# Performance work log

Hardware: AMD Instinct MI355X
Metric: run time of the kernel (lower is better)

## Reference

```python
import jax, jax.numpy as jnp
import numpy as np

N_NODES = 200000


def setup_inputs() -> dict:
    key = jax.random.key(0)
    k1, k2, k3, k4 = jax.random.split(key, 4)
    x = jax.random.normal(k1, (N_NODES, 16), dtype=jnp.float32)
    edge_index = jax.random.randint(k2, (2, 2400000), 0, N_NODES, dtype=jnp.int64)
    W1 = jax.random.normal(k3, (16, 32), dtype=jnp.float32) * 0.25
    b1 = jnp.zeros((32,), dtype=jnp.float32)
    W2 = jax.random.normal(k4, (32, 32), dtype=jnp.float32) * 0.18
    b2 = jnp.zeros((32,), dtype=jnp.float32)
    return {"x": x, "edge_index": edge_index, "W1": W1, "b1": b1, "W2": W2, "b2": b2}


def _gcn_norm(edge_index, n_nodes):
    # Add self-loops (GCNConv default) and compute symmetric normalization
    # norm[e] = deg(src)^-1/2 * deg(dst)^-1/2 over A + I.
    loop = jnp.arange(n_nodes, dtype=edge_index.dtype)
    src = jnp.concatenate([edge_index[0], loop])
    dst = jnp.concatenate([edge_index[1], loop])
    deg = jax.ops.segment_sum(jnp.ones_like(dst, dtype=jnp.float32), dst,
                              num_segments=n_nodes)
    dinv = jax.lax.rsqrt(deg)  # deg >= 1 thanks to self-loops
    norm = dinv[src] * dinv[dst]  # [E + N]
    return src, dst, norm


def _gcn_layer(h, src, dst, norm, W, b, n_nodes):
    m = h @ W                      # [N, out] dense transform first (fewer bytes moved)
    agg = jax.ops.segment_sum(m[src] * norm[:, None], dst, num_segments=n_nodes)
    return agg + b


def reference(x, edge_index, W1, b1, W2, b2):
    n = x.shape[0]
    src, dst, norm = _gcn_norm(edge_index, n)
    h = jax.nn.relu(_gcn_layer(x, src, dst, norm, W1, b1, n))
    out = _gcn_layer(h, src, dst, norm, W2, b2, n)
    return out
```

## Files before the change

### kernel.cpp

```cpp
#include <hip/hip_runtime.h>

#define TPB 256
#define BEB 2048
#define SEB 2048
#define PEB 8192
#define NS_SH 7
#define NS (1 << NS_SH)
#define CAP3 4096

__global__ void k_detect_i64(const unsigned int* __restrict__ ei, int E,
                             int* __restrict__ flag, int* __restrict__ cum) {
  __shared__ int nz;
  if (threadIdx.x == 0) nz = 0;
  if (threadIdx.x < 7) cum[threadIdx.x] = 0;
  __syncthreads();
  int step = E / 4096;
  if (step < 1) step = 1;
  for (int t = threadIdx.x; t < 4096; t += blockDim.x) {
    long long pos = 1 + 2LL * (long long)t * step;
    if (pos < 2LL * (long long)E && ei[pos] != 0u) atomicAdd(&nz, 1);
  }
  __syncthreads();
  if (threadIdx.x == 0) *flag = (nz == 0) ? 1 : 0;
}

__device__ __forceinline__ int load_idx(const void* __restrict__ p, long long pos,
                                        int is64) {
  if (is64) return (int)(((const long long*)p)[pos]);
  return ((const int*)p)[pos];
}

__global__ void k_zero_i(int* __restrict__ p, int n) {
  int i = blockIdx.x * blockDim.x + threadIdx.x;
  if (i < n) p[i] = 0;
}

__global__ void k_count8(const void* __restrict__ ei, const int* __restrict__ flag,
                         int* __restrict__ cum, int E, int Nc) {
  int is64 = *flag;
  int c[7] = {0, 0, 0, 0, 0, 0, 0};
  int stride = gridDim.x * blockDim.x;
  for (int e = blockIdx.x * blockDim.x + threadIdx.x; e < E; e += stride) {
    int d = load_idx(ei, (long long)E + e, is64);
#pragma unroll
    for (int k = 0; k < 7; ++k) c[k] += (d < (k + 1) * Nc) ? 1 : 0;
  }
#pragma unroll
  for (int k = 0; k < 7; ++k)
#pragma unroll
    for (int off = 32; off >= 1; off >>= 1) c[k] += __shfl_xor(c[k], off);
  __shared__ int red[4][7];
  int lane = threadIdx.x & 63, wid = threadIdx.x >> 6;
  if (lane == 0) {
#pragma unroll
    for (int k = 0; k < 7; ++k) red[wid][k] = c[k];
  }
  __syncthreads();
  if (threadIdx.x < 7) {
    int s = red[0][threadIdx.x] + red[1][threadIdx.x] +
            red[2][threadIdx.x] + red[3][threadIdx.x];
    if (s) atomicAdd(&cum[threadIdx.x], s);
  }
}

__global__ void k_cbase(const int* __restrict__ cum, int* __restrict__ ccnt,
                        int* __restrict__ cbase, int* __restrict__ gtail, int E) {
  if (threadIdx.x == 0) {
    int prev = 0, acc = 0;
    for (int g = 0; g < 8; ++g) {
      int cg = ((g < 7) ? cum[g] : E) - prev;
      prev = (g < 7) ? cum[g] : E;
      ccnt[g] = cg;
      cbase[g] = acc;
      gtail[g] = acc;
      acc += cg;
    }
  }
}

__global__ void k_bucket(const void* __restrict__ ei, const int* __restrict__ flag,
                         int* __restrict__ gtail, unsigned long long* __restrict__ pair,
                         int E, int Nc) {
  __shared__ int sd[BEB], ss[BEB];
  __shared__ int bbase[8], cur[8];
  __shared__ int red[4][7];
  int is64 = *flag;
  int base = blockIdx.x * BEB;
  int cnt = min(BEB, E - base);
  int c[7] = {0, 0, 0, 0, 0, 0, 0};
  for (int i = threadIdx.x; i < cnt; i += TPB) {
    int e = base + i;
    int d = load_idx(ei, (long long)E + e, is64);
    int s = load_idx(ei, e, is64);
    sd[i] = d;
    ss[i] = s;
#pragma unroll
    for (int k = 0; k < 7; ++k) c[k] += (d < (k + 1) * Nc) ? 1 : 0;
  }
#pragma unroll
  for (int k = 0; k < 7; ++k)
#pragma unroll
    for (int off = 32; off >= 1; off >>= 1) c[k] += __shfl_xor(c[k], off);
  int lane = threadIdx.x & 63, wid = threadIdx.x >> 6;
  if (lane == 0) {
#pragma unroll
    for (int k = 0; k < 7; ++k) red[wid][k] = c[k];
  }
  __syncthreads();
  if (threadIdx.x < 8) {
    int g = threadIdx.x;
    int hi = (g < 7) ? (red[0][g] + red[1][g] + red[2][g] + red[3][g]) : cnt;
    int lo = (g > 0) ? (red[0][g - 1] + red[1][g - 1] + red[2][g - 1] + red[3][g - 1]) : 0;
    bbase[g] = atomicAdd(&gtail[g], hi - lo);
    cur[g] = 0;
  }
  __syncthreads();
  int trips = (cnt + TPB - 1) / TPB;
  unsigned long long lt = (1ULL << lane) - 1ULL;
  for (int t = 0; t < trips; ++t) {
    int i = t * TPB + threadIdx.x;
    bool act = i < cnt;
    int d = act ? sd[i] : 0;
    int s = act ? ss[i] : 0;
    int g = 0;
#pragma unroll
    for (int k = 1; k <= 7; ++k) g += (d >= k * Nc) ? 1 : 0;
    unsigned long long m0 = __ballot(act && g == 0);
    unsigned long long m1 = __ballot(act && g == 1);
    unsigned long long m2 = __ballot(act && g == 2);
    unsigned long long m3 = __ballot(act && g == 3);
    unsigned long long m4 = __ballot(act && g == 4);
    unsigned long long m5 = __ballot(act && g == 5);
    unsigned long long m6 = __ballot(act && g == 6);
    unsigned long long m7 = __ballot(act && g == 7);
    int wb = 0;
    if (lane < 8) {
      unsigned long long mm =
          lane < 4 ? (lane < 2 ? (lane == 0 ? m0 : m1) : (lane == 2 ? m2 : m3))
                   : (lane < 6 ? (lane == 4 ? m4 : m5) : (lane == 6 ? m6 : m7));
      wb = atomicAdd(&cur[lane], (int)__popcll(mm));
    }
    int mybase = __shfl(wb, g);
    unsigned long long mk =
        g < 4 ? (g < 2 ? (g == 0 ? m0 : m1) : (g == 2 ? m2 : m3))
              : (g < 6 ? (g == 4 ? m4 : m5) : (g == 6 ? m6 : m7));
    int rank = (int)__popcll(mk & lt);
    if (act) {
      int pos = bbase[g] + mybase + rank;
      unsigned long long pk =
          ((unsigned long long)(unsigned)s << 32) | (unsigned)d;
      __builtin_nontemporal_store(pk, &pair[pos]);
    }
  }
}

__global__ void k_scnt(const int* __restrict__ cbase, const int* __restrict__ ccnt,
                       const int2* __restrict__ pair, int* __restrict__ scnt,
                       int nsb_c, int Nc) {
  __shared__ int hist[256];
  for (int t = threadIdx.x; t < nsb_c; t += TPB) hist[t] = 0;
  __syncthreads();
  int g = blockIdx.x & 7, seg = blockIdx.x >> 3;
  int cnt = ccnt[g];
  int base = seg * SEB;
  if (base < cnt) {
    int lim = min(base + SEB, cnt);
    const int2* pp = pair + cbase[g];
    int lo = g * Nc;
    for (int i = base + threadIdx.x; i < lim; i += TPB)
      atomicAdd(&hist[(pp[i].x - lo) >> NS_SH], 1);
  }
  __syncthreads();
  for (int t = threadIdx.x; t < nsb_c; t += TPB)
    if (hist[t]) atomicAdd(&scnt[g * nsb_c + t], hist[t]);
}

__global__ void k_sbase(const int* __restrict__ scnt, int* __restrict__ sbase,
                        int* __restrict__ stail, int nsb) {
  __shared__ int p[1024];
  int t = threadIdx.x;
  int i0 = 2 * t, i1 = 2 * t + 1;
  int v0 = (i0 < nsb) ? scnt[i0] : 0;
  int v1 = (i1 < nsb) ? scnt[i1] : 0;
  p[t] = v0 + v1;
  __syncthreads();
#pragma unroll
  for (int off = 1; off < 1024; off <<= 1) {
    int u = (t >= off) ? p[t - off] : 0;
    __syncthreads();
    p[t] += u;
    __syncthreads();
  }
  int excl = p[t] - (v0 + v1);
  if (i0 < nsb) { sbase[i0] = excl; stail[i0] = excl; }
  if (i1 < nsb) { sbase[i1] = excl + v0; stail[i1] = excl + v0; }
}

__global__ void k_place2(const int* __restrict__ cbase, const int* __restrict__ ccnt,
                         const unsigned long long* __restrict__ pair,
                         int* __restrict__ stail, unsigned long long* __restrict__ pair2,
                         int nsb_c, int Nc) {
  __shared__ unsigned long long sorted[PEB];
  __shared__ int hist[256], bb[256], gb[256], cur[256];
  int g = blockIdx.x & 7, seg = blockIdx.x >> 3;
  int cnt = ccnt[g];
  int base = seg * PEB;
  if (base >= cnt) return;
  int lim = min(base + PEB, cnt);
  int lo = g * Nc;
  const unsigned long long* pp = pair + cbase[g];
  for (int t = threadIdx.x; t < 256; t += TPB) hist[t] = 0;
  __syncthreads();
  for (int i = base + threadIdx.x; i < lim; i += TPB) {
    int d = (int)(unsigned)(pp[i] & 0xffffffffULL);
    atomicAdd(&hist[(d - lo) >> NS_SH], 1);
  }
  __syncthreads();
  {
    int t = threadIdx.x;
    int v = hist[t];
    bb[t] = v;
    __syncthreads();
#pragma unroll
    for (int off = 1; off < 256; off <<= 1) {
      int u = (t >= off) ? bb[t - off] : 0;
      __syncthreads();
      bb[t] += u;
      __syncthreads();
    }
    bb[t] -= v;
  }
  for (int t = threadIdx.x; t < nsb_c; t += TPB) {
    gb[t] = hist[t] ? atomicAdd(&stail[g * nsb_c + t], hist[t]) : 0;
    cur[t] = 0;
  }
  __syncthreads();
  for (int i = base + threadIdx.x; i < lim; i += TPB) {
    unsigned long long pk = pp[i];
    int d = (int)(unsigned)(pk & 0xffffffffULL);
    int sb = (d - lo) >> NS_SH;
    int r = atomicAdd(&cur[sb], 1);
    sorted[bb[sb] + r] = pk;
  }
  __syncthreads();
  int n = lim - base;
  for (int i = threadIdx.x; i < n; i += TPB) {
    unsigned long long pk = sorted[i];
    int d = (int)(unsigned)(pk & 0xffffffffULL);
    int sb = (d - lo) >> NS_SH;
    pair2[gb[sb] + (i - bb[sb])] = pk;
  }
}

__global__ void k_hist3(const int* __restrict__ scnt, const int* __restrict__ sbase,
                        const int2* __restrict__ pair2, int* __restrict__ degi,
                        int nsb_c, int Nc, int N) {
  __shared__ int hist[NS];
  int sb = blockIdx.x;
  int g = sb / nsb_c, lsb = sb - g * nsb_c;
  int n0 = g * Nc + (lsb << NS_SH);
  int nn = min(NS, min(Nc - (lsb << NS_SH), N - n0));
  if (nn <= 0) return;
  for (int t = threadIdx.x; t < NS; t += TPB) hist[t] = 0;
  __syncthreads();
  int cnt = scnt[sb];
  const int2* pp = pair2 + sbase[sb];
  for (int i = threadIdx.x; i < cnt; i += TPB) atomicAdd(&hist[pp[i].x - n0], 1);
  __syncthreads();
  for (int t = threadIdx.x; t < nn; t += TPB) degi[n0 + t] = hist[t];
}

__global__ void k_scan1(const int* __restrict__ degi, int* __restrict__ incl,
                        int* __restrict__ bsums, int n) {
  __shared__ int s[TPB];
  int i = blockIdx.x * TPB + threadIdx.x;
  int v = (i < n) ? degi[i] : 0;
  s[threadIdx.x] = v;
  __syncthreads();
#pragma unroll
  for (int off = 1; off < TPB; off <<= 1) {
    int t = (threadIdx.x >= off) ? s[threadIdx.x - off] : 0;
    __syncthreads();
    s[threadIdx.x] += t;
    __syncthreads();
  }
  if (i < n) incl[i] = s[threadIdx.x];
  if (threadIdx.x == TPB - 1) bsums[blockIdx.x] = s[TPB - 1];
}

__global__ void k_scan2(int* __restrict__ bsums, int nb) {
  __shared__ int s[1024];
  int t = threadIdx.x;
  int v = (t < nb) ? bsums[t] : 0;
  s[t] = v;
  __syncthreads();
#pragma unroll
  for (int off = 1; off < 1024; off <<= 1) {
    int u = (t >= off) ? s[t - off] : 0;
    __syncthreads();
    s[t] += u;
    __syncthreads();
  }
  if (t < nb) bsums[t] = s[t] - v;
}

__global__ void k_finalize(const int* __restrict__ degi, const int* __restrict__ incl,
                           const int* __restrict__ bsums, int* __restrict__ cursor,
                           float* __restrict__ dinv, int4* __restrict__ meta, int n) {
  int i = blockIdx.x * TPB + threadIdx.x;
  if (i >= n) return;
  int dg = degi[i];
  int st = bsums[blockIdx.x] + incl[i] - dg;
  float di = rsqrtf((float)(dg + 1));
  cursor[i] = st;
  dinv[i] = di;
  meta[i] = make_int4(st, dg, __float_as_int(di), 0);
}

__global__ void k_sort3(const int* __restrict__ scnt, const int* __restrict__ sbase,
                        const int2* __restrict__ pair2, const int4* __restrict__ meta,
                        int* __restrict__ cursor, int* __restrict__ ssrc,
                        int nsb_c, int Nc, int N) {
  __shared__ int st[NS];
  __shared__ int curi[NS];
  __shared__ int ss[CAP3];
  int sb = blockIdx.x;
  int g = sb / nsb_c, lsb = sb - g * nsb_c;
  int n0 = g * Nc + (lsb << NS_SH);
  int nn = min(NS, min(Nc - (lsb << NS_SH), N - n0));
  if (nn <= 0) return;
  int cnt = scnt[sb];
  if (cnt == 0) return;
  const int2* pp = pair2 + sbase[sb];
  if (cnt <= CAP3) {
    for (int t = threadIdx.x; t < nn; t += TPB) {
      st[t] = meta[n0 + t].x;
      curi[t] = 0;
    }
    __syncthreads();
    int base0 = st[0];
    for (int i = threadIdx.x; i < cnt; i += TPB) {
      int2 pr = pp[i];
      int l = pr.x - n0;
      int r = atomicAdd(&curi[l], 1);
      ss[(st[l] - base0) + r] = pr.y;
    }
    __syncthreads();
    for (int i = threadIdx.x; i < cnt; i += TPB) ssrc[base0 + i] = ss[i];
  } else {
    for (int i = threadIdx.x; i < cnt; i += TPB) {
      int2 pr = pp[i];
      int pos = atomicAdd(&cursor[pr.x], 1);
      ssrc[pos] = pr.y;
    }
  }
}

__global__ void k_prescale16(const float* __restrict__ x, const float* __restrict__ dinv,
                             float* __restrict__ gx, int n4) {
  int gid = blockIdx.x * blockDim.x + threadIdx.x;
  if (gid >= n4) return;
  int i = gid >> 2;
  float di = dinv[i];
  float4 v = reinterpret_cast<const float4*>(x)[gid];
  v.x *= di; v.y *= di; v.z *= di; v.w *= di;
  reinterpret_cast<float4*>(gx)[gid] = v;
}

template <int CH>
__global__ void k_gatherT(const int4* __restrict__ meta, const int* __restrict__ ssrc,
                          const float* __restrict__ v, float* __restrict__ outp, int n) {
  int gid = blockIdx.x * blockDim.x + threadIdx.x;
  int dst = gid >> 2;
  int q = gid & 3;
  if (dst >= n) return;
  int4 md = meta[dst];
  int s0 = md.x;
  int dg = md.y;
  float dd = __int_as_float(md.z);
  size_t o0 = (size_t)q * 4;
  size_t o1 = o0 + 16;
  const float* rd = v + (size_t)dst * CH;
  float4 a0 = *reinterpret_cast<const float4*>(rd + o0);
  float4 a1;
  if (CH == 32) a1 = *reinterpret_cast<const float4*>(rd + o1);
  int j = 0;
  for (; j + 2 <= dg; j += 2) {
    int s1 = __builtin_nontemporal_load(&ssrc[s0 + j]);
    int s2 = __builtin_nontemporal_load(&ssrc[s0 + j + 1]);
    const float* r1 = v + (size_t)s1 * CH;
    const float* r2 = v + (size_t)s2 * CH;
    float4 v0 = *reinterpret_cast<const float4*>(r1 + o0);
    float4 w0 = *reinterpret_cast<const float4*>(r2 + o0);
    a0.x += v0.x + w0.x; a0.y += v0.y + w0.y; a0.z += v0.z + w0.z; a0.w += v0.w + w0.w;
    if (CH == 32) {
      float4 v1 = *reinterpret_cast<const float4*>(r1 + o1);
      float4 w1 = *reinterpret_cast<const float4*>(r2 + o1);
      a1.x += v1.x + w1.x; a1.y += v1.y + w1.y; a1.z += v1.z + w1.z; a1.w += v1.w + w1.w;
    }
  }
  if (j < dg) {
    int s1 = __builtin_nontemporal_load(&ssrc[s0 + j]);
    const float* r1 = v + (size_t)s1 * CH;
    float4 v0 = *reinterpret_cast<const float4*>(r1 + o0);
    a0.x += v0.x; a0.y += v0.y; a0.z += v0.z; a0.w += v0.w;
    if (CH == 32) {
      float4 v1 = *reinterpret_cast<const float4*>(r1 + o1);
      a1.x += v1.x; a1.y += v1.y; a1.z += v1.z; a1.w += v1.w;
    }
  }
  a0.x *= dd; a0.y *= dd; a0.z *= dd; a0.w *= dd;
  float* wr = outp + (size_t)dst * CH;
  *reinterpret_cast<float4*>(wr + o0) = a0;
  if (CH == 32) {
    a1.x *= dd; a1.y *= dd; a1.z *= dd; a1.w *= dd;
    *reinterpret_cast<float4*>(wr + o1) = a1;
  }
}

template <int IN, int OUT, bool RELU, bool PRESCALE>
__global__ void k_transform(const float* __restrict__ h, const float* __restrict__ W,
                            const float* __restrict__ b, const float* __restrict__ dinv,
                            float* __restrict__ outp, int n) {
  __shared__ float sW[IN * OUT];
  __shared__ float sB[OUT];
  for (int t = threadIdx.x; t < IN * OUT; t += blockDim.x) sW[t] = W[t];
  if (threadIdx.x < OUT) sB[threadIdx.x] = b[threadIdx.x];
  __syncthreads();
  int i = blockIdx.x * blockDim.x + threadIdx.x;
  if (i >= n) return;
  float xr[IN];
  const float4* hp = reinterpret_cast<const float4*>(h + (size_t)i * IN);
#pragma unroll
  for (int k4 = 0; k4 < IN / 4; ++k4) {
    float4 v = hp[k4];
    xr[k4 * 4 + 0] = v.x; xr[k4 * 4 + 1] = v.y;
    xr[k4 * 4 + 2] = v.z; xr[k4 * 4 + 3] = v.w;
  }
  float acc[OUT];
#pragma unroll
  for (int c = 0; c < OUT; ++c) acc[c] = sB[c];
#pragma unroll
  for (int k = 0; k < IN; ++k) {
    float xv = xr[k];
#pragma unroll
    for (int c = 0; c < OUT; ++c) acc[c] = fmaf(xv, sW[k * OUT + c], acc[c]);
  }
  float di = PRESCALE ? dinv[i] : 1.0f;
  float4* mp = reinterpret_cast<float4*>(outp + (size_t)i * OUT);
#pragma unroll
  for (int c4 = 0; c4 < OUT / 4; ++c4) {
    float4 o;
    o.x = acc[c4 * 4 + 0]; o.y = acc[c4 * 4 + 1];
    o.z = acc[c4 * 4 + 2]; o.w = acc[c4 * 4 + 3];
    if (RELU) {
      o.x = fmaxf(o.x, 0.0f); o.y = fmaxf(o.y, 0.0f);
      o.z = fmaxf(o.z, 0.0f); o.w = fmaxf(o.w, 0.0f);
    }
    if (PRESCALE) { o.x *= di; o.y *= di; o.z *= di; o.w *= di; }
    mp[c4] = o;
  }
}

extern "C" void kernel_launch(void* const* d_in, const int* in_sizes, int n_in,
                              void* d_out, int out_size, void* d_ws, size_t ws_size,
                              hipStream_t stream) {
  const float* x  = (const float*)d_in[0];
  const void*  ei = d_in[1];
  const float* W1 = (const float*)d_in[2];
  const float* b1 = (const float*)d_in[3];
  const float* W2 = (const float*)d_in[4];
  const float* b2 = (const float*)d_in[5];
  float* out = (float*)d_out;

  const int N = in_sizes[0] / 16;
  const int E = in_sizes[1] / 2;
  const int Nc = (N + 7) / 8;
  const int nsb_c = (Nc + NS - 1) / NS;
  const int NSB = 8 * nsb_c;

  char* p = (char*)d_ws;
  auto alloc = [&](size_t bytes) {
    char* r = p;
    p += (bytes + 255) & ~(size_t)255;
    return r;
  };
  int*   flag   = (int*)alloc(4);
  float* dinv   = (float*)alloc((size_t)N * 4);
  int*   degi   = (int*)alloc((size_t)N * 4);
  int*   incl   = (int*)alloc((size_t)N * 4);
  int*   cursor = (int*)alloc((size_t)N * 4);
  int4*  meta   = (int4*)alloc((size_t)N * 16);
  int*   bsums  = (int*)alloc(4096);
  int*   cum    = (int*)alloc(64);
  int*   ccnt   = (int*)alloc(64);
  int*   cbase  = (int*)alloc(64);
  int*   gtail  = (int*)alloc(64);
  int*   scnt   = (int*)alloc((size_t)NSB * 4);
  int*   sbase  = (int*)alloc((size_t)NSB * 4);
  int*   stail  = (int*)alloc((size_t)NSB * 4);
  int*   ssrc   = (int*)alloc((size_t)E * 4);
  float* bufA   = (float*)alloc((size_t)N * 32 * 4);
  float* bufB   = (float*)alloc((size_t)N * 32 * 4);
  unsigned long long* pairW  = (unsigned long long*)bufA;
  const int2*         pairR  = (const int2*)bufA;
  unsigned long long* pair2W = (unsigned long long*)bufB;
  const int2*         pair2R = (const int2*)bufB;
  float* gx   = bufA;
  float* agg1 = bufB;
  float* gh   = bufA;
  float* agg2 = bufB;

  const int gN  = (N + TPB - 1) / TPB;
  const int gN4 = (N * 4 + TPB - 1) / TPB;
  const int gBk = (E + BEB - 1) / BEB;
  const int gSc = ((E + SEB - 1) / SEB) * 8;
  const int gP2 = ((E + PEB - 1) / PEB) * 8;

  k_detect_i64<<<1, TPB, 0, stream>>>((const unsigned int*)ei, E, flag, cum);
  k_count8<<<512, TPB, 0, stream>>>(ei, flag, cum, E, Nc);
  k_cbase<<<1, 64, 0, stream>>>(cum, ccnt, cbase, gtail, E);
  k_zero_i<<<(NSB + TPB - 1) / TPB, TPB, 0, stream>>>(scnt, NSB);
  k_bucket<<<gBk, TPB, 0, stream>>>(ei, flag, gtail, pairW, E, Nc);
  k_scnt<<<gSc, TPB, 0, stream>>>(cbase, ccnt, pairR, scnt, nsb_c, Nc);
  k_sbase<<<1, 1024, 0, stream>>>(scnt, sbase, stail, NSB);
  k_place2<<<gP2, TPB, 0, stream>>>(cbase, ccnt, pairW, stail, pair2W, nsb_c, Nc);
  k_hist3<<<NSB, TPB, 0, stream>>>(scnt, sbase, pair2R, degi, nsb_c, Nc, N);
  k_scan1<<<gN, TPB, 0, stream>>>(degi, incl, bsums, N);
  k_scan2<<<1, 1024, 0, stream>>>(bsums, gN);
  k_finalize<<<gN, TPB, 0, stream>>>(degi, incl, bsums, cursor, dinv, meta, N);
  k_sort3<<<NSB, TPB, 0, stream>>>(scnt, sbase, pair2R, meta, cursor, ssrc, nsb_c, Nc, N);
  k_prescale16<<<gN4, TPB, 0, stream>>>(x, dinv, gx, N * 4);
  k_gatherT<16><<<gN4, TPB, 0, stream>>>(meta, ssrc, gx, agg1, N);
  k_transform<16, 32, true, true><<<gN, TPB, 0, stream>>>(agg1, W1, b1, dinv, gh, N);
  k_gatherT<32><<<gN4, TPB, 0, stream>>>(meta, ssrc, gh, agg2, N);
  k_transform<32, 32, false, false><<<gN, TPB, 0, stream>>>(agg2, W2, b2, dinv, out, N);
}
```

Measured before the change: 339.8 us.

## Fuse CSR build into per-superblock gather with packed 32-bit edge records

Edge pairs are packed into a single 32-bit word (source shifted left, plus the local destination offset within a 128-node superblock), which halves the pair2 traffic. The separate histogram, scan, finalize and sort3 kernels are removed. Degree counting and x prescaling are fused into one k_prep kernel, and each gather kernel now sorts its superblock's edges in LDS before aggregating, so no global CSR is built. Both gather layers redo the local sort, and superblocks with more than 2560 edges fall back to slow per-channel global atomics.

After: 320.7 us. 5.6% less time.

```diff
diff --git a/kernel.cpp b/kernel.cpp
--- a/kernel.cpp
+++ b/kernel.cpp
@@ -1,12 +1,13 @@
 #include <hip/hip_runtime.h>
 
 #define TPB 256
+#define TPG 512
 #define BEB 2048
 #define SEB 2048
 #define PEB 8192
 #define NS_SH 7
 #define NS (1 << NS_SH)
-#define CAP3 4096
+#define CAP 2560
 
 __global__ void k_detect_i64(const unsigned int* __restrict__ ei, int E,
                              int* __restrict__ flag, int* __restrict__ cum) {
@@ -198,9 +199,9 @@
 
 __global__ void k_place2(const int* __restrict__ cbase, const int* __restrict__ ccnt,
                          const unsigned long long* __restrict__ pair,
-                         int* __restrict__ stail, unsigned long long* __restrict__ pair2,
+                         int* __restrict__ stail, int* __restrict__ pair2,
                          int nsb_c, int Nc) {
-  __shared__ unsigned long long sorted[PEB];
+  __shared__ int sorted[PEB];
   __shared__ int hist[256], bb[256], gb[256], cur[256];
   int g = blockIdx.x & 7, seg = blockIdx.x >> 3;
   int cnt = ccnt[g];
@@ -238,183 +239,155 @@
   for (int i = base + threadIdx.x; i < lim; i += TPB) {
     unsigned long long pk = pp[i];
     int d = (int)(unsigned)(pk & 0xffffffffULL);
-    int sb = (d - lo) >> NS_SH;
+    int rel = d - lo;
+    int sb = rel >> NS_SH;
+    int packed = ((int)(pk >> 32) << NS_SH) | (rel & (NS - 1));
     int r = atomicAdd(&cur[sb], 1);
-    sorted[bb[sb] + r] = pk;
+    sorted[bb[sb] + r] = packed;
   }
   __syncthreads();
   int n = lim - base;
   for (int i = threadIdx.x; i < n; i += TPB) {
-    unsigned long long pk = sorted[i];
-    int d = (int)(unsigned)(pk & 0xffffffffULL);
-    int sb = (d - lo) >> NS_SH;
-    pair2[gb[sb] + (i - bb[sb])] = pk;
-  }
-}
-
-__global__ void k_hist3(const int* __restrict__ scnt, const int* __restrict__ sbase,
-                        const int2* __restrict__ pair2, int* __restrict__ degi,
-                        int nsb_c, int Nc, int N) {
+    int packed = sorted[i];
+    int loi = 0, hii = nsb_c;
+    while (hii - loi > 1) {
+      int mid = (loi + hii) >> 1;
+      if (bb[mid] <= i) loi = mid; else hii = mid;
+    }
+    pair2[gb[loi] + (i - bb[loi])] = packed;
+  }
+}
+
+__global__ void k_prep(const int* __restrict__ scnt, const int* __restrict__ sbase,
+                       const int* __restrict__ pair2, const float* __restrict__ x,
+                       float* __restrict__ dinv, float* __restrict__ gx,
+                       int nsb_c, int Nc, int N) {
   __shared__ int hist[NS];
+  __shared__ float sdi[NS];
   int sb = blockIdx.x;
   int g = sb / nsb_c, lsb = sb - g * nsb_c;
   int n0 = g * Nc + (lsb << NS_SH);
   int nn = min(NS, min(Nc - (lsb << NS_SH), N - n0));
   if (nn <= 0) return;
-  for (int t = threadIdx.x; t < NS; t += TPB) hist[t] = 0;
+  for (int t = threadIdx.x; t < NS; t += TPG) hist[t] = 0;
   __syncthreads();
   int cnt = scnt[sb];
-  const int2* pp = pair2 + sbase[sb];
-  for (int i = threadIdx.x; i < cnt; i += TPB) atomicAdd(&hist[pp[i].x - n0], 1);
-  __syncthreads();
-  for (int t = threadIdx.x; t < nn; t += TPB) degi[n0 + t] = hist[t];
-}
-
-__global__ void k_scan1(const int* __restrict__ degi, int* __restrict__ incl,
-                        int* __restrict__ bsums, int n) {
-  __shared__ int s[TPB];
-  int i = blockIdx.x * TPB + threadIdx.x;
-  int v = (i < n) ? degi[i] : 0;
-  s[threadIdx.x] = v;
-  __syncthreads();
-#pragma unroll
-  for (int off = 1; off < TPB; off <<= 1) {
-    int t = (threadIdx.x >= off) ? s[threadIdx.x - off] : 0;
-    __syncthreads();
-    s[threadIdx.x] += t;
-    __syncthreads();
-  }
-  if (i < n) incl[i] = s[threadIdx.x];
-  if (threadIdx.x == TPB - 1) bsums[blockIdx.x] = s[TPB - 1];
-}
-
-__global__ void k_scan2(int* __restrict__ bsums, int nb) {
-  __shared__ int s[1024];
-  int t = threadIdx.x;
-  int v = (t < nb) ? bsums[t] : 0;
-  s[t] = v;
-  __syncthreads();
-#pragma unroll
-  for (int off = 1; off < 1024; off <<= 1) {
-    int u = (t >= off) ? s[t - off] : 0;
-    __syncthreads();
-    s[t] += u;
-    __syncthreads();
-  }
-  if (t < nb) bsums[t] = s[t] - v;
-}
-
-__global__ void k_finalize(const int* __restrict__ degi, const int* __restrict__ incl,
-                           const int* __restrict__ bsums, int* __restrict__ cursor,
-                           float* __restrict__ dinv, int4* __restrict__ meta, int n) {
-  int i = blockIdx.x * TPB + threadIdx.x;
-  if (i >= n) return;
-  int dg = degi[i];
-  int st = bsums[blockIdx.x] + incl[i] - dg;
-  float di = rsqrtf((float)(dg + 1));
-  cursor[i] = st;
-  dinv[i] = di;
-  meta[i] = make_int4(st, dg, __float_as_int(di), 0);
-}
-
-__global__ void k_sort3(const int* __restrict__ scnt, const int* __restrict__ sbase,
-                        const int2* __restrict__ pair2, const int4* __restrict__ meta,
-                        int* __restrict__ cursor, int* __restrict__ ssrc,
-                        int nsb_c, int Nc, int N) {
-  __shared__ int st[NS];
-  __shared__ int curi[NS];
-  __shared__ int ss[CAP3];
+  const int* pp = pair2 + sbase[sb];
+  for (int i = threadIdx.x; i < cnt; i += TPG)
+    atomicAdd(&hist[pp[i] & (NS - 1)], 1);
+  __syncthreads();
+  for (int t = threadIdx.x; t < nn; t += TPG) {
+    float di = rsqrtf((float)(hist[t] + 1));
+    sdi[t] = di;
+    dinv[n0 + t] = di;
+  }
+  __syncthreads();
+  int tot = nn * 16;
+  const float* xb = x + (size_t)n0 * 16;
+  float* gb_ = gx + (size_t)n0 * 16;
+  for (int idx = threadIdx.x; idx < tot; idx += TPG)
+    gb_[idx] = xb[idx] * sdi[idx >> 4];
+}
+
+template <int CH>
+__global__ void k_gatherF(const int* __restrict__ scnt, const int* __restrict__ sbase,
+                          const int* __restrict__ pair2, const float* __restrict__ dinv,
+                          const float* __restrict__ v, float* __restrict__ agg,
+                          int nsb_c, int Nc, int N) {
+  __shared__ int hist[NS], bb[NS], cur[NS];
+  __shared__ int sl[CAP];
   int sb = blockIdx.x;
   int g = sb / nsb_c, lsb = sb - g * nsb_c;
   int n0 = g * Nc + (lsb << NS_SH);
   int nn = min(NS, min(Nc - (lsb << NS_SH), N - n0));
   if (nn <= 0) return;
   int cnt = scnt[sb];
-  if (cnt == 0) return;
-  const int2* pp = pair2 + sbase[sb];
-  if (cnt <= CAP3) {
-    for (int t = threadIdx.x; t < nn; t += TPB) {
-      st[t] = meta[n0 + t].x;
-      curi[t] = 0;
-    }
-    __syncthreads();
-    int base0 = st[0];
-    for (int i = threadIdx.x; i < cnt; i += TPB) {
-      int2 pr = pp[i];
-      int l = pr.x - n0;
-      int r = atomicAdd(&curi[l], 1);
-      ss[(st[l] - base0) + r] = pr.y;
-    }
-    __syncthreads();
-    for (int i = threadIdx.x; i < cnt; i += TPB) ssrc[base0 + i] = ss[i];
+  const int* pp = pair2 + sbase[sb];
+  int tid = threadIdx.x;
+  if (cnt <= CAP) {
+    for (int t = tid; t < NS; t += TPG) { hist[t] = 0; cur[t] = 0; }
+    __syncthreads();
+    for (int i = tid; i < cnt; i += TPG) atomicAdd(&hist[pp[i] & (NS - 1)], 1);
+    __syncthreads();
+    if (tid < NS) bb[tid] = hist[tid];
+    __syncthreads();
+#pragma unroll
+    for (int off = 1; off < NS; off <<= 1) {
+      int u = (tid < NS && tid >= off) ? bb[tid - off] : 0;
+      __syncthreads();
+      if (tid < NS) bb[tid] += u;
+      __syncthreads();
+    }
+    if (tid < NS) bb[tid] -= hist[tid];
+    __syncthreads();
+    for (int i = tid; i < cnt; i += TPG) {
+      int pk = pp[i];
+      int l = pk & (NS - 1);
+      int r = atomicAdd(&cur[l], 1);
+      sl[bb[l] + r] = pk >> NS_SH;
+    }
+    __syncthreads();
+    int grp = tid >> 2, q = tid & 3;
+    if (grp < nn) {
+      int dst = n0 + grp;
+      float dd = dinv[dst];
+      int s0 = bb[grp], dg = hist[grp];
+      size_t o0 = (size_t)q * 4;
+      size_t o1 = o0 + 16;
+      const float* rd = v + (size_t)dst * CH;
+      float4 a0 = *reinterpret_cast<const float4*>(rd + o0);
+      float4 a1;
+      if (CH == 32) a1 = *reinterpret_cast<const float4*>(rd + o1);
+      int j = 0;
+      for (; j + 2 <= dg; j += 2) {
+        int s1 = sl[s0 + j];
+        int s2 = sl[s0 + j + 1];
+        const float* r1 = v + (size_t)s1 * CH;
+        const float* r2 = v + (size_t)s2 * CH;
+        float4 v0 = *reinterpret_cast<const float4*>(r1 + o0);
+        float4 w0 = *reinterpret_cast<const float4*>(r2 + o0);
+        a0.x += v0.x + w0.x; a0.y += v0.y + w0.y;
+        a0.z += v0.z + w0.z; a0.w += v0.w + w0.w;
+        if (CH == 32) {
+          float4 v1 = *reinterpret_cast<const float4*>(r1 + o1);
+          float4 w1 = *reinterpret_cast<const float4*>(r2 + o1);
+          a1.x += v1.x + w1.x; a1.y += v1.y + w1.y;
+          a1.z += v1.z + w1.z; a1.w += v1.w + w1.w;
+        }
+      }
+      if (j < dg) {
+        int s1 = sl[s0 + j];
+        const float* r1 = v + (size_t)s1 * CH;
+        float4 v0 = *reinterpret_cast<const float4*>(r1 + o0);
+        a0.x += v0.x; a0.y += v0.y; a0.z += v0.z; a0.w += v0.w;
+        if (CH == 32) {
+          float4 v1 = *reinterpret_cast<const float4*>(r1 + o1);
+          a1.x += v1.x; a1.y += v1.y; a1.z += v1.z; a1.w += v1.w;
+        }
+      }
+      a0.x *= dd; a0.y *= dd; a0.z *= dd; a0.w *= dd;
+      float* wr = agg + (size_t)dst * CH;
+      *reinterpret_cast<float4*>(wr + o0) = a0;
+      if (CH == 32) {
+        a1.x *= dd; a1.y *= dd; a1.z *= dd; a1.w *= dd;
+        *reinterpret_cast<float4*>(wr + o1) = a1;
+      }
+    }
   } else {
-    for (int i = threadIdx.x; i < cnt; i += TPB) {
-      int2 pr = pp[i];
-      int pos = atomicAdd(&cursor[pr.x], 1);
-      ssrc[pos] = pr.y;
-    }
-  }
-}
-
-__global__ void k_prescale16(const float* __restrict__ x, const float* __restrict__ dinv,
-                             float* __restrict__ gx, int n4) {
-  int gid = blockIdx.x * blockDim.x + threadIdx.x;
-  if (gid >= n4) return;
-  int i = gid >> 2;
-  float di = dinv[i];
-  float4 v = reinterpret_cast<const float4*>(x)[gid];
-  v.x *= di; v.y *= di; v.z *= di; v.w *= di;
-  reinterpret_cast<float4*>(gx)[gid] = v;
-}
-
-template <int CH>
-__global__ void k_gatherT(const int4* __restrict__ meta, const int* __restrict__ ssrc,
-                          const float* __restrict__ v, float* __restrict__ outp, int n) {
-  int gid = blockIdx.x * blockDim.x + threadIdx.x;
-  int dst = gid >> 2;
-  int q = gid & 3;
-  if (dst >= n) return;
-  int4 md = meta[dst];
-  int s0 = md.x;
-  int dg = md.y;
-  float dd = __int_as_float(md.z);
-  size_t o0 = (size_t)q * 4;
-  size_t o1 = o0 + 16;
-  const float* rd = v + (size_t)dst * CH;
-  float4 a0 = *reinterpret_cast<const float4*>(rd + o0);
-  float4 a1;
-  if (CH == 32) a1 = *reinterpret_cast<const float4*>(rd + o1);
-  int j = 0;
-  for (; j + 2 <= dg; j += 2) {
-    int s1 = __builtin_nontemporal_load(&ssrc[s0 + j]);
-    int s2 = __builtin_nontemporal_load(&ssrc[s0 + j + 1]);
-    const float* r1 = v + (size_t)s1 * CH;
-    const float* r2 = v + (size_t)s2 * CH;
-    float4 v0 = *reinterpret_cast<const float4*>(r1 + o0);
-    float4 w0 = *reinterpret_cast<const float4*>(r2 + o0);
-    a0.x += v0.x + w0.x; a0.y += v0.y + w0.y; a0.z += v0.z + w0.z; a0.w += v0.w + w0.w;
-    if (CH == 32) {
-      float4 v1 = *reinterpret_cast<const float4*>(r1 + o1);
-      float4 w1 = *reinterpret_cast<const float4*>(r2 + o1);
-      a1.x += v1.x + w1.x; a1.y += v1.y + w1.y; a1.z += v1.z + w1.z; a1.w += v1.w + w1.w;
-    }
-  }
-  if (j < dg) {
-    int s1 = __builtin_nontemporal_load(&ssrc[s0 + j]);
-    const float* r1 = v + (size_t)s1 * CH;
-    float4 v0 = *reinterpret_cast<const float4*>(r1 + o0);
-    a0.x += v0.x; a0.y += v0.y; a0.z += v0.z; a0.w += v0.w;
-    if (CH == 32) {
-      float4 v1 = *reinterpret_cast<const float4*>(r1 + o1);
-      a1.x += v1.x; a1.y += v1.y; a1.z += v1.z; a1.w += v1.w;
-    }
-  }
-  a0.x *= dd; a0.y *= dd; a0.z *= dd; a0.w *= dd;
-  float* wr = outp + (size_t)dst * CH;
-  *reinterpret_cast<float4*>(wr + o0) = a0;
-  if (CH == 32) {
-    a1.x *= dd; a1.y *= dd; a1.z *= dd; a1.w *= dd;
-    *reinterpret_cast<float4*>(wr + o1) = a1;
+    for (int idx = tid; idx < nn * CH; idx += TPG) {
+      int l = idx / CH, c = idx - l * CH;
+      float dd = dinv[n0 + l];
+      agg[(size_t)(n0 + l) * CH + c] = v[(size_t)(n0 + l) * CH + c] * dd;
+    }
+    __syncthreads();
+    for (int i = tid; i < cnt; i += TPG) {
+      int pk = pp[i];
+      int l = pk & (NS - 1);
+      int s = pk >> NS_SH;
+      float dd = dinv[n0 + l];
+      for (int c = 0; c < CH; ++c)
+        atomicAdd(&agg[(size_t)(n0 + l) * CH + c], v[(size_t)s * CH + c] * dd);
+    }
   }
 }
 
@@ -485,34 +458,26 @@
     p += (bytes + 255) & ~(size_t)255;
     return r;
   };
-  int*   flag   = (int*)alloc(4);
-  float* dinv   = (float*)alloc((size_t)N * 4);
-  int*   degi   = (int*)alloc((size_t)N * 4);
-  int*   incl   = (int*)alloc((size_t)N * 4);
-  int*   cursor = (int*)alloc((size_t)N * 4);
-  int4*  meta   = (int4*)alloc((size_t)N * 16);
-  int*   bsums  = (int*)alloc(4096);
-  int*   cum    = (int*)alloc(64);
-  int*   ccnt   = (int*)alloc(64);
-  int*   cbase  = (int*)alloc(64);
-  int*   gtail  = (int*)alloc(64);
-  int*   scnt   = (int*)alloc((size_t)NSB * 4);
-  int*   sbase  = (int*)alloc((size_t)NSB * 4);
-  int*   stail  = (int*)alloc((size_t)NSB * 4);
-  int*   ssrc   = (int*)alloc((size_t)E * 4);
-  float* bufA   = (float*)alloc((size_t)N * 32 * 4);
-  float* bufB   = (float*)alloc((size_t)N * 32 * 4);
-  unsigned long long* pairW  = (unsigned long long*)bufA;
-  const int2*         pairR  = (const int2*)bufA;
-  unsigned long long* pair2W = (unsigned long long*)bufB;
-  const int2*         pair2R = (const int2*)bufB;
+  int*   flag  = (int*)alloc(4);
+  float* dinv  = (float*)alloc((size_t)N * 4);
+  int*   cum   = (int*)alloc(64);
+  int*   ccnt  = (int*)alloc(64);
+  int*   cbase = (int*)alloc(64);
+  int*   gtail = (int*)alloc(64);
+  int*   scnt  = (int*)alloc((size_t)NSB * 4);
+  int*   sbase = (int*)alloc((size_t)NSB * 4);
+  int*   stail = (int*)alloc((size_t)NSB * 4);
+  int*   pair2 = (int*)alloc((size_t)E * 4);
+  float* bufA  = (float*)alloc((size_t)N * 32 * 4);
+  float* bufC  = (float*)alloc((size_t)N * 32 * 4);
+  unsigned long long* pairW = (unsigned long long*)bufA;
+  const int2*         pairR = (const int2*)bufA;
   float* gx   = bufA;
-  float* agg1 = bufB;
-  float* gh   = bufA;
-  float* agg2 = bufB;
+  float* agg1 = bufA + (size_t)N * 16;
+  float* gh   = bufC;
+  float* agg2 = bufA;
 
   const int gN  = (N + TPB - 1) / TPB;
-  const int gN4 = (N * 4 + TPB - 1) / TPB;
   const int gBk = (E + BEB - 1) / BEB;
   const int gSc = ((E + SEB - 1) / SEB) * 8;
   const int gP2 = ((E + PEB - 1) / PEB) * 8;
@@ -524,15 +489,10 @@
   k_bucket<<<gBk, TPB, 0, stream>>>(ei, flag, gtail, pairW, E, Nc);
   k_scnt<<<gSc, TPB, 0, stream>>>(cbase, ccnt, pairR, scnt, nsb_c, Nc);
   k_sbase<<<1, 1024, 0, stream>>>(scnt, sbase, stail, NSB);
-  k_place2<<<gP2, TPB, 0, stream>>>(cbase, ccnt, pairW, stail, pair2W, nsb_c, Nc);
-  k_hist3<<<NSB, TPB, 0, stream>>>(scnt, sbase, pair2R, degi, nsb_c, Nc, N);
-  k_scan1<<<gN, TPB, 0, stream>>>(degi, incl, bsums, N);
-  k_scan2<<<1, 1024, 0, stream>>>(bsums, gN);
-  k_finalize<<<gN, TPB, 0, stream>>>(degi, incl, bsums, cursor, dinv, meta, N);
-  k_sort3<<<NSB, TPB, 0, stream>>>(scnt, sbase, pair2R, meta, cursor, ssrc, nsb_c, Nc, N);
-  k_prescale16<<<gN4, TPB, 0, stream>>>(x, dinv, gx, N * 4);
-  k_gatherT<16><<<gN4, TPB, 0, stream>>>(meta, ssrc, gx, agg1, N);
+  k_place2<<<gP2, TPB, 0, stream>>>(cbase, ccnt, pairW, stail, pair2, nsb_c, Nc);
+  k_prep<<<NSB, TPG, 0, stream>>>(scnt, sbase, pair2, x, dinv, gx, nsb_c, Nc, N);
+  k_gatherF<16><<<NSB, TPG, 0, stream>>>(scnt, sbase, pair2, dinv, gx, agg1, nsb_c, Nc, N);
   k_transform<16, 32, true, true><<<gN, TPB, 0, stream>>>(agg1, W1, b1, dinv, gh, N);
-  k_gatherT<32><<<gN4, TPB, 0, stream>>>(meta, ssrc, gh, agg2, N);
+  k_gatherF<32><<<NSB, TPG, 0, stream>>>(scnt, sbase, pair2, dinv, gh, agg2, nsb_c, Nc, N);
   k_transform<32, 32, false, false><<<gN, TPB, 0, stream>>>(agg2, W2, b2, dinv, out, N);
 }
```
